# Performance work log

Hardware: AMD Instinct MI355X
Metric: run time of the kernel (lower is better)

Reference implementation:

```python
import jax, jax.numpy as jnp
import numpy as np

HIDDEN = 768
NUM_HEADS = 12
HEAD_SIZE = HIDDEN // NUM_HEADS
LN_EPS = 1e-5


def setup_inputs() -> dict:
    key = jax.random.key(0)
    ks = jax.random.split(key, 10)
    B, S, H = 2, 4096, HIDDEN
    std = 1.0 / np.sqrt(H)
    inp = {
        "hidden_states": jax.random.normal(ks[0], (B, S, H), dtype=jnp.float32),
        "attention_mask": jnp.ones((B, S), dtype=jnp.float32),
        "Wq": jax.random.normal(ks[1], (H, H), dtype=jnp.float32) * std,
        "bq": jnp.zeros((H,), dtype=jnp.float32),
        "Wk": jax.random.normal(ks[2], (H, H), dtype=jnp.float32) * std,
        "bk": jnp.zeros((H,), dtype=jnp.float32),
        "Wv": jax.random.normal(ks[3], (H, H), dtype=jnp.float32) * std,
        "bv": jnp.zeros((H,), dtype=jnp.float32),
        "Wo": jax.random.normal(ks[4], (H, H), dtype=jnp.float32) * std,
        "bo": jnp.zeros((H,), dtype=jnp.float32),
        "ln_gamma": jnp.ones((H,), dtype=jnp.float32),
        "ln_beta": jnp.zeros((H,), dtype=jnp.float32),
    }
    return inp


def _split_heads(x):
    # [B, S, H] -> [B, nH, S, hd]
    B, S, _ = x.shape
    return x.reshape(B, S, NUM_HEADS, HEAD_SIZE).transpose(0, 2, 1, 3)


def reference(hidden_states, attention_mask, Wq, bq, Wk, bk, Wv, bv, Wo, bo, ln_gamma, ln_beta):
    # QKV projections (torch Linear: x @ W.T + b; here W is stored as [in, out])
    q = _split_heads(hidden_states @ Wq + bq)
    k = _split_heads(hidden_states @ Wk + bk)
    v = _split_heads(hidden_states @ Wv + bv)

    scores = jnp.einsum("bhqd,bhkd->bhqk", q, k) / jnp.sqrt(jnp.float32(HEAD_SIZE))
    # additive mask: (1 - mask) * -10000, broadcast over heads and query positions
    scores = scores + (1.0 - attention_mask)[:, None, None, :] * -10000.0
    probs = jax.nn.softmax(scores, axis=-1)  # dropout_prob = 0 -> identity

    ctx = jnp.einsum("bhqk,bhkd->bhqd", probs, v)
    B, _, S, _ = ctx.shape
    ctx = ctx.transpose(0, 2, 1, 3).reshape(B, S, HIDDEN)

    out = ctx @ Wo + bo
    resid = out + hidden_states
    mu = jnp.mean(resid, axis=-1, keepdims=True)
    var = jnp.var(resid, axis=-1, keepdims=True)
    return (resid - mu) * jax.lax.rsqrt(var + LN_EPS) * ln_gamma + ln_beta
```

## Files before the change

### kernel.cpp

```cpp
#include <hip/hip_runtime.h>
#include <hip/hip_bf16.h>

#define HID 768
#define NHEADS 12
#define HDIM 64
#define SEQ 4096
#define BB 2
#define MTOT (BB * SEQ)

typedef __attribute__((ext_vector_type(8))) short bf16x8;
typedef __attribute__((ext_vector_type(16))) float f32x16;

#define LOG2E 1.4426950408889634f

__device__ inline unsigned pack2bf(float a, float b) {
    __hip_bfloat162 h = __float22bfloat162_rn(float2{a, b});
    return *(unsigned*)&h;
}

__global__ __launch_bounds__(256) void cast_x_kernel(
    const float* __restrict__ X, __hip_bfloat16* __restrict__ Xb)
{
    const size_t i = ((size_t)blockIdx.x * 256 + threadIdx.x) * 8;
    const float4 x0 = *(const float4*)(X + i);
    const float4 x1 = *(const float4*)(X + i + 4);
    unsigned u[4];
    u[0] = pack2bf(x0.x, x0.y);
    u[1] = pack2bf(x0.z, x0.w);
    u[2] = pack2bf(x1.x, x1.y);
    u[3] = pack2bf(x1.z, x1.w);
    *(uint4*)(Xb + i) = *(uint4*)u;
}

__global__ __launch_bounds__(256) void pack_w_kernel(
    const float* __restrict__ Wq, const float* __restrict__ Wk,
    const float* __restrict__ Wv, const float* __restrict__ Wo,
    __hip_bfloat16* __restrict__ Wt)
{
    const int z = blockIdx.z;
    const float* __restrict__ W = (z == 0) ? Wq : (z == 1) ? Wk : (z == 2) ? Wv : Wo;
    const int in0  = blockIdx.x * 64;
    const int out0 = blockIdx.y * 64;
    const int t = threadIdx.x;

    __shared__ float T[64][65];
#pragma unroll
    for (int i = 0; i < 4; ++i) {
        const int idx = t + 256 * i;
        const int row = idx >> 4;
        const int c4  = (idx & 15) << 2;
        const float4 v = *(const float4*)(W + (size_t)(in0 + row) * HID + out0 + c4);
        T[row][c4 + 0] = v.x; T[row][c4 + 1] = v.y;
        T[row][c4 + 2] = v.z; T[row][c4 + 3] = v.w;
    }
    __syncthreads();

    const int o  = t >> 2;
    const int cb = (t & 3) << 4;
    __hip_bfloat16 tmp[16];
#pragma unroll
    for (int k = 0; k < 16; ++k)
        tmp[k] = __float2bfloat16(T[cb + k][o]);
    __hip_bfloat16* __restrict__ dst =
        Wt + (size_t)(z * HID + out0 + o) * HID + in0 + cb;
    *(uint4*)(dst)     = *(uint4*)(&tmp[0]);
    *(uint4*)(dst + 8) = *(uint4*)(&tmp[8]);
}

__global__ __launch_bounds__(256) void qkv_mfma_kernel(
    const __hip_bfloat16* __restrict__ Xb, const __hip_bfloat16* __restrict__ Wt,
    const float* __restrict__ bq, const float* __restrict__ bk,
    const float* __restrict__ bv,
    __hip_bfloat16* __restrict__ Qo, __hip_bfloat16* __restrict__ Ko,
    __hip_bfloat16* __restrict__ Vo)
{
    const int nblk = blockIdx.x;
    const int z  = nblk / 6;
    const int f0 = (nblk % 6) * 128;
    const int n0 = nblk * 128;
    const int m0 = blockIdx.y * 128;

    const float* __restrict__ bias = (z == 0) ? bq : (z == 1) ? bk : bv;

    const int t    = threadIdx.x;
    const int w    = t >> 6;
    const int lane = t & 63;
    const int col  = lane & 31;
    const int g    = lane >> 5;
    const int wm   = w & 1;
    const int wn   = w >> 1;

    __shared__ __hip_bfloat16 smem[2 * 128 * 72];
    __hip_bfloat16 (*As)[72] = (__hip_bfloat16(*)[72])smem;
    __hip_bfloat16 (*Bs)[72] = (__hip_bfloat16(*)[72])(smem + 128 * 72);

    f32x16 acc[2][2];
#pragma unroll
    for (int mt = 0; mt < 2; ++mt)
#pragma unroll
        for (int nt = 0; nt < 2; ++nt)
#pragma unroll
            for (int r = 0; r < 16; ++r) acc[mt][nt][r] = 0.f;

    for (int k0 = 0; k0 < HID; k0 += 64) {
        __syncthreads();
#pragma unroll
        for (int i = 0; i < 4; ++i) {
            const int idx = t + 256 * i;
            const int row = idx >> 3;
            const int c8  = (idx & 7) << 3;
            *(uint4*)&As[row][c8] = *(const uint4*)(Xb + (size_t)(m0 + row) * HID + k0 + c8);
            *(uint4*)&Bs[row][c8] = *(const uint4*)(Wt + (size_t)(n0 + row) * HID + k0 + c8);
        }
        __syncthreads();
#pragma unroll
        for (int kh = 0; kh < 4; ++kh) {
            const int ko = 16 * kh + 8 * g;
            const bf16x8 a0 = *(const bf16x8*)&As[64 * wm + col][ko];
            const bf16x8 a1 = *(const bf16x8*)&As[64 * wm + 32 + col][ko];
            const bf16x8 b0 = *(const bf16x8*)&Bs[64 * wn + col][ko];
            const bf16x8 b1 = *(const bf16x8*)&Bs[64 * wn + 32 + col][ko];
            acc[0][0] = __builtin_amdgcn_mfma_f32_32x32x16_bf16(a0, b0, acc[0][0], 0, 0, 0);
            acc[0][1] = __builtin_amdgcn_mfma_f32_32x32x16_bf16(a0, b1, acc[0][1], 0, 0, 0);
            acc[1][0] = __builtin_amdgcn_mfma_f32_32x32x16_bf16(a1, b0, acc[1][0], 0, 0, 0);
            acc[1][1] = __builtin_amdgcn_mfma_f32_32x32x16_bf16(a1, b1, acc[1][1], 0, 0, 0);
        }
    }

    if (z < 2) {
        __hip_bfloat16* __restrict__ Out = (z == 0) ? Qo : Ko;
        const int h = (f0 >> 6) + wn;
#pragma unroll
        for (int mt = 0; mt < 2; ++mt)
#pragma unroll
            for (int nt = 0; nt < 2; ++nt) {
                const int d = 32 * nt + col;
                const float bsv = bias[f0 + 64 * wn + d];
#pragma unroll
                for (int r = 0; r < 16; ++r) {
                    const int m = m0 + 64 * wm + 32 * mt + (r & 3) + 8 * (r >> 2) + 4 * g;
                    const int b = m >> 12;
                    const int s = m & (SEQ - 1);
                    Out[(((size_t)(b * NHEADS + h)) * SEQ + s) * HDIM + d] =
                        __float2bfloat16(acc[mt][nt][r] + bsv);
                }
            }
    } else {
        __syncthreads();
        __hip_bfloat16 (*Ts)[136] = (__hip_bfloat16(*)[136])smem;
#pragma unroll
        for (int mt = 0; mt < 2; ++mt)
#pragma unroll
            for (int nt = 0; nt < 2; ++nt) {
                const int nloc = 64 * wn + 32 * nt + col;
                const float bsv = bias[f0 + nloc];
#pragma unroll
                for (int rg = 0; rg < 4; ++rg) {
                    const int mbase = 64 * wm + 32 * mt + 8 * rg + 4 * g;
                    unsigned pu[2];
                    pu[0] = pack2bf(acc[mt][nt][4 * rg + 0] + bsv,
                                    acc[mt][nt][4 * rg + 1] + bsv);
                    pu[1] = pack2bf(acc[mt][nt][4 * rg + 2] + bsv,
                                    acc[mt][nt][4 * rg + 3] + bsv);
                    *(uint2*)&Ts[nloc][mbase] = *(uint2*)pu;
                }
            }
        __syncthreads();
        const int nloc = t >> 1;
        const int half = t & 1;
        const int hh = (f0 >> 6) + (nloc >> 6);
        const int d  = nloc & 63;
        const int bb = m0 >> 12;
        const int s0 = m0 & (SEQ - 1);
        __hip_bfloat16* __restrict__ dst =
            Vo + (((size_t)(bb * NHEADS + hh)) * HDIM + d) * SEQ + s0 + 64 * half;
        const __hip_bfloat16* srcp = &Ts[nloc][64 * half];
#pragma unroll
        for (int j = 0; j < 8; ++j)
            *(uint4*)(dst + 8 * j) = *(const uint4*)(srcp + 8 * j);
    }
}

typedef __attribute__((ext_vector_type(2))) unsigned uswap2;

__global__ __launch_bounds__(256, 2) void attn_kernel(
    const __hip_bfloat16* __restrict__ Qb, const __hip_bfloat16* __restrict__ Kb,
    const __hip_bfloat16* __restrict__ Vt, const float* __restrict__ mask,
    __hip_bfloat16* __restrict__ Op, float* __restrict__ lp)
{
    const int bh = blockIdx.y;
    const int b  = bh / NHEADS;
    const int h  = bh - b * NHEADS;
    const int kspan = SEQ / gridDim.z;
    const int kbeg  = blockIdx.z * kspan;

    const int t    = threadIdx.x;
    const int w    = t >> 6;
    const int lane = t & 63;
    const int col  = lane & 31;
    const int g    = lane >> 5;
    const int qw   = blockIdx.x * 256 + 64 * w;

    __shared__ __hip_bfloat16 Ksb[2][64][64];
    __shared__ __hip_bfloat16 Vsb[2][64][64];
    __shared__ float madd[2048];

    const __hip_bfloat16* __restrict__ Qh = Qb + (size_t)bh * SEQ * HDIM;
    const __hip_bfloat16* __restrict__ Kh = Kb + (size_t)bh * SEQ * HDIM;
    const __hip_bfloat16* __restrict__ Vh = Vt + (size_t)bh * HDIM * SEQ;

    for (int j = t; j < kspan; j += 256)
        madd[j] = (1.0f - mask[b * SEQ + kbeg + j]) * (-10000.0f * LOG2E);

    const int r0  = t >> 3;
    const int csw = (((t & 7) ^ (r0 & 7)) << 3);

#define STAGE(BUF, KT) do {                                                        \
    const __hip_bfloat16* gk0_ = Kh + (size_t)((KT) + r0) * HDIM + csw;            \
    const __hip_bfloat16* gk1_ = Kh + (size_t)((KT) + r0 + 32) * HDIM + csw;       \
    const __hip_bfloat16* gv0_ = Vh + (size_t)r0 * SEQ + (KT) + csw;               \
    const __hip_bfloat16* gv1_ = Vh + (size_t)(r0 + 32) * SEQ + (KT) + csw;        \
    __hip_bfloat16* lk_ = &Ksb[BUF][0][0] + w * 512;                               \
    __hip_bfloat16* lv_ = &Vsb[BUF][0][0] + w * 512;                               \
    __builtin_amdgcn_global_load_lds(                                              \
        (const __attribute__((address_space(1))) unsigned*)gk0_,                   \
        (__attribute__((address_space(3))) unsigned*)lk_, 16, 0, 0);               \
    __builtin_amdgcn_global_load_lds(                                              \
        (const __attribute__((address_space(1))) unsigned*)gk1_,                   \
        (__attribute__((address_space(3))) unsigned*)(lk_ + 2048), 16, 0, 0);      \
    __builtin_amdgcn_global_load_lds(                                              \
        (const __attribute__((address_space(1))) unsigned*)gv0_,                   \
        (__attribute__((address_space(3))) unsigned*)lv_, 16, 0, 0);               \
    __builtin_amdgcn_global_load_lds(                                              \
        (const __attribute__((address_space(1))) unsigned*)gv1_,                   \
        (__attribute__((address_space(3))) unsigned*)(lv_ + 2048), 16, 0, 0);      \
} while (0)

    bf16x8 bq[2][4];
#pragma unroll
    for (int mt = 0; mt < 2; ++mt)
#pragma unroll
        for (int kh = 0; kh < 4; ++kh)
            bq[mt][kh] = *(const bf16x8*)(Qh + (size_t)(qw + 32 * mt + col) * HDIM
                                          + 16 * kh + 8 * g);

    f32x16 O[2][2];
    float lac[2] = {0.f, 0.f};
#pragma unroll
    for (int mt = 0; mt < 2; ++mt)
#pragma unroll
        for (int dt = 0; dt < 2; ++dt)
#pragma unroll
            for (int r = 0; r < 16; ++r) O[mt][dt][r] = 0.f;

    const float kscale = 0.125f * LOG2E;

#define ATTN_TILE(BUF, KT0) do {                                                   \
    f32x16 St[2][2];                                                               \
    _Pragma("unroll")                                                              \
    for (int mt = 0; mt < 2; ++mt)                                                 \
        _Pragma("unroll")                                                          \
        for (int nt = 0; nt < 2; ++nt)                                             \
            _Pragma("unroll")                                                      \
            for (int r = 0; r < 16; ++r) St[mt][nt][r] = 0.f;                      \
    _Pragma("unroll")                                                              \
    for (int kh = 0; kh < 4; ++kh) {                                               \
        const int sc = ((2 * kh + g) ^ (col & 7)) << 3;                            \
        const bf16x8 ak0 = *(const bf16x8*)&Ksb[BUF][col][sc];                     \
        const bf16x8 ak1 = *(const bf16x8*)&Ksb[BUF][32 + col][sc];                \
        St[0][0] = __builtin_amdgcn_mfma_f32_32x32x16_bf16(ak0, bq[0][kh], St[0][0], 0, 0, 0); \
        St[1][0] = __builtin_amdgcn_mfma_f32_32x32x16_bf16(ak0, bq[1][kh], St[1][0], 0, 0, 0); \
        St[0][1] = __builtin_amdgcn_mfma_f32_32x32x16_bf16(ak1, bq[0][kh], St[0][1], 0, 0, 0); \
        St[1][1] = __builtin_amdgcn_mfma_f32_32x32x16_bf16(ak1, bq[1][kh], St[1][1], 0, 0, 0); \
    }                                                                              \
    _Pragma("unroll")                                                              \
    for (int mt = 0; mt < 2; ++mt) {                                               \
        unsigned g4x[2][4], g4y[2][4];                                             \
        _Pragma("unroll")                                                          \
        for (int nt = 0; nt < 2; ++nt) {                                           \
            _Pragma("unroll")                                                      \
            for (int b4 = 0; b4 < 4; ++b4) {                                       \
                const float4 mm = *(const float4*)&madd[(KT0) + 32 * nt + 8 * b4 + 4 * g]; \
                const float p0 = __builtin_amdgcn_exp2f(fmaf(St[mt][nt][4 * b4 + 0], kscale, mm.x)); \
                const float p1 = __builtin_amdgcn_exp2f(fmaf(St[mt][nt][4 * b4 + 1], kscale, mm.y)); \
                const float p2 = __builtin_amdgcn_exp2f(fmaf(St[mt][nt][4 * b4 + 2], kscale, mm.z)); \
                const float p3 = __builtin_amdgcn_exp2f(fmaf(St[mt][nt][4 * b4 + 3], kscale, mm.w)); \
                lac[mt] += (p0 + p1) + (p2 + p3);                                  \
                g4x[nt][b4] = pack2bf(p0, p1);                                     \
                g4y[nt][b4] = pack2bf(p2, p3);                                     \
            }                                                                      \
        }                                                                          \
        _Pragma("unroll")                                                          \
        for (int kh = 0; kh < 4; ++kh) {                                           \
            const int nt  = kh >> 1;                                               \
            const int khl = kh & 1;                                                \
            union { unsigned u[4]; bf16x8 v; } au;                                 \
            ATTN_PTRANS(au, g4x[nt][2 * khl], g4x[nt][2 * khl + 1],                \
                            g4y[nt][2 * khl], g4y[nt][2 * khl + 1]);               \
            const int sc = ((2 * kh + g) ^ (col & 7)) << 3;                        \
            const bf16x8 bv0 = *(const bf16x8*)&Vsb[BUF][col][sc];                 \
            const bf16x8 bv1 = *(const bf16x8*)&Vsb[BUF][32 + col][sc];            \
            O[mt][0] = __builtin_amdgcn_mfma_f32_32x32x16_bf16(au.v, bv0, O[mt][0], 0, 0, 0); \
            O[mt][1] = __builtin_amdgcn_mfma_f32_32x32x16_bf16(au.v, bv1, O[mt][1], 0, 0, 0); \
        }                                                                          \
    }                                                                              \
} while (0)

#if __has_builtin(__builtin_amdgcn_permlane32_swap)
#define ATTN_PTRANS(au, lox, hix, loy, hiy) do {                                   \
    uswap2 sx_ = __builtin_amdgcn_permlane32_swap((lox), (hix), false, false);     \
    uswap2 sy_ = __builtin_amdgcn_permlane32_swap((loy), (hiy), false, false);     \
    au.u[0] = sx_[0]; au.u[1] = sy_[0]; au.u[2] = sx_[1]; au.u[3] = sy_[1];        \
} while (0)
#else
#define ATTN_PTRANS(au, lox, hix, loy, hiy) do {                                   \
    const unsigned sxv_ = g ? (lox) : (hix);                                       \
    const unsigned syv_ = g ? (loy) : (hiy);                                       \
    const unsigned rx_ = (unsigned)__shfl_xor((int)sxv_, 32, 64);                  \
    const unsigned ry_ = (unsigned)__shfl_xor((int)syv_, 32, 64);                  \
    if (g) { au.u[0] = rx_;   au.u[1] = ry_;   au.u[2] = (hix); au.u[3] = (hiy); } \
    else   { au.u[0] = (lox); au.u[1] = (loy); au.u[2] = rx_;   au.u[3] = ry_;  }  \
} while (0)
#endif

    STAGE(0, kbeg);
    __syncthreads();

    for (int kt0 = 0; kt0 < kspan; kt0 += 128) {
        STAGE(1, kbeg + kt0 + 64);
        ATTN_TILE(0, kt0);
        __syncthreads();
        if (kt0 + 128 < kspan) STAGE(0, kbeg + kt0 + 128);
        ATTN_TILE(1, kt0 + 64);
        __syncthreads();
    }
#undef STAGE
#undef ATTN_TILE
#undef ATTN_PTRANS

    const size_t opbase = (size_t)blockIdx.z * ((size_t)MTOT * HID);
#pragma unroll
    for (int mt = 0; mt < 2; ++mt) {
        const float l = lac[mt] + __shfl_xor(lac[mt], 32, 64);
        if (g == 0)
            lp[((size_t)blockIdx.z * (BB * NHEADS) + bh) * SEQ + qw + 32 * mt + col] = l;
#pragma unroll
        for (int dt = 0; dt < 2; ++dt)
#pragma unroll
            for (int r = 0; r < 16; ++r) {
                const int q = qw + 32 * mt + (r & 3) + 8 * (r >> 2) + 4 * g;
                const int d = 32 * dt + col;
                Op[opbase + ((size_t)b * SEQ + q) * HID + h * HDIM + d] =
                    __float2bfloat16(O[mt][dt][r]);
            }
    }
}

__global__ __launch_bounds__(256) void combine_kernel(
    const __hip_bfloat16* __restrict__ Op, const float* __restrict__ lp,
    __hip_bfloat16* __restrict__ Ctx, int KS)
{
    const size_t i = ((size_t)blockIdx.x * 256 + threadIdx.x) * 8;
    const int n   = (int)(i % HID);
    const int row = (int)(i / HID);
    const int h = n >> 6;
    const int b = row >> 12;
    const int q = row & (SEQ - 1);
    const int bh = b * NHEADS + h;

    float denom = 0.f;
    float o[8] = {};
    for (int kz = 0; kz < KS; ++kz) {
        denom += lp[((size_t)kz * (BB * NHEADS) + bh) * SEQ + q];
        uint4 u = *(const uint4*)(Op + (size_t)kz * ((size_t)MTOT * HID) + i);
        const __hip_bfloat16* e = (const __hip_bfloat16*)&u;
#pragma unroll
        for (int j = 0; j < 8; ++j) o[j] += __bfloat162float(e[j]);
    }
    const float inv = 1.0f / denom;
    unsigned u[4];
#pragma unroll
    for (int j = 0; j < 4; ++j)
        u[j] = pack2bf(o[2 * j] * inv, o[2 * j + 1] * inv);
    *(uint4*)(Ctx + i) = *(uint4*)u;
}

__global__ __launch_bounds__(256) void out_mfma_kernel(
    const __hip_bfloat16* __restrict__ Cb, const __hip_bfloat16* __restrict__ Wto,
    const float* __restrict__ bo, const float* __restrict__ X,
    float* __restrict__ Resid)
{
    const int n0 = blockIdx.x * 128;
    const int m0 = blockIdx.y * 128;

    const int t    = threadIdx.x;
    const int w    = t >> 6;
    const int lane = t & 63;
    const int col  = lane & 31;
    const int g    = lane >> 5;
    const int wm   = w & 1;
    const int wn   = w >> 1;

    __shared__ __hip_bfloat16 As[128][72];
    __shared__ __hip_bfloat16 Bs[128][72];

    f32x16 acc[2][2];
#pragma unroll
    for (int mt = 0; mt < 2; ++mt)
#pragma unroll
        for (int nt = 0; nt < 2; ++nt)
#pragma unroll
            for (int r = 0; r < 16; ++r) acc[mt][nt][r] = 0.f;

    for (int k0 = 0; k0 < HID; k0 += 64) {
        __syncthreads();
#pragma unroll
        for (int i = 0; i < 4; ++i) {
            const int idx = t + 256 * i;
            const int row = idx >> 3;
            const int c8  = (idx & 7) << 3;
            *(uint4*)&As[row][c8] = *(const uint4*)(Cb  + (size_t)(m0 + row) * HID + k0 + c8);
            *(uint4*)&Bs[row][c8] = *(const uint4*)(Wto + (size_t)(n0 + row) * HID + k0 + c8);
        }
        __syncthreads();
#pragma unroll
        for (int kh = 0; kh < 4; ++kh) {
            const int ko = 16 * kh + 8 * g;
            const bf16x8 a0 = *(const bf16x8*)&As[64 * wm + col][ko];
            const bf16x8 a1 = *(const bf16x8*)&As[64 * wm + 32 + col][ko];
            const bf16x8 b0 = *(const bf16x8*)&Bs[64 * wn + col][ko];
            const bf16x8 b1 = *(const bf16x8*)&Bs[64 * wn + 32 + col][ko];
            acc[0][0] = __builtin_amdgcn_mfma_f32_32x32x16_bf16(a0, b0, acc[0][0], 0, 0, 0);
            acc[0][1] = __builtin_amdgcn_mfma_f32_32x32x16_bf16(a0, b1, acc[0][1], 0, 0, 0);
            acc[1][0] = __builtin_amdgcn_mfma_f32_32x32x16_bf16(a1, b0, acc[1][0], 0, 0, 0);
            acc[1][1] = __builtin_amdgcn_mfma_f32_32x32x16_bf16(a1, b1, acc[1][1], 0, 0, 0);
        }
    }

#pragma unroll
    for (int mt = 0; mt < 2; ++mt)
#pragma unroll
        for (int nt = 0; nt < 2; ++nt) {
            const int n = n0 + 64 * wn + 32 * nt + col;
            const float bsv = bo[n];
#pragma unroll
            for (int r = 0; r < 16; ++r) {
                const int m = m0 + 64 * wm + 32 * mt + (r & 3) + 8 * (r >> 2) + 4 * g;
                Resid[(size_t)m * HID + n] = acc[mt][nt][r] + bsv + X[(size_t)m * HID + n];
            }
        }
}

__global__ __launch_bounds__(256) void ln_kernel(
    const float* __restrict__ Rin, const float* __restrict__ gamma,
    const float* __restrict__ beta, float* __restrict__ Out)
{
    const int row = blockIdx.x;
    const int t   = threadIdx.x;
    const float* __restrict__ x = Rin + (size_t)row * HID;

    const float v0 = x[t];
    const float v1 = x[t + 256];
    const float v2 = x[t + 512];
    float s  = v0 + v1 + v2;
    float s2 = v0 * v0 + v1 * v1 + v2 * v2;
#pragma unroll
    for (int off = 32; off; off >>= 1) {
        s  += __shfl_xor(s,  off, 64);
        s2 += __shfl_xor(s2, off, 64);
    }
    __shared__ float rs[4], rs2[4];
    const int w = t >> 6, lane = t & 63;
    if (lane == 0) { rs[w] = s; rs2[w] = s2; }
    __syncthreads();
    const float tot  = rs[0] + rs[1] + rs[2] + rs[3];
    const float tot2 = rs2[0] + rs2[1] + rs2[2] + rs2[3];
    const float mu   = tot * (1.0f / HID);
    const float var  = tot2 * (1.0f / HID) - mu * mu;
    const float rsig = rsqrtf(var + 1e-5f);

    float* __restrict__ y = Out + (size_t)row * HID;
    y[t]       = (v0 - mu) * rsig * gamma[t]       + beta[t];
    y[t + 256] = (v1 - mu) * rsig * gamma[t + 256] + beta[t + 256];
    y[t + 512] = (v2 - mu) * rsig * gamma[t + 512] + beta[t + 512];
}

extern "C" void kernel_launch(void* const* d_in, const int* in_sizes, int n_in,
                              void* d_out, int out_size, void* d_ws, size_t ws_size,
                              hipStream_t stream)
{
    const float* X     = (const float*)d_in[0];
    const float* mask  = (const float*)d_in[1];
    const float* Wq    = (const float*)d_in[2];
    const float* bq    = (const float*)d_in[3];
    const float* Wk    = (const float*)d_in[4];
    const float* bk    = (const float*)d_in[5];
    const float* Wv    = (const float*)d_in[6];
    const float* bv    = (const float*)d_in[7];
    const float* Wo    = (const float*)d_in[8];
    const float* bo    = (const float*)d_in[9];
    const float* gamma = (const float*)d_in[10];
    const float* beta  = (const float*)d_in[11];
    float* out = (float*)d_out;

    const size_t N = (size_t)MTOT * HID;
    const size_t WTE = (size_t)4 * HID * HID;

    char* p = (char*)d_ws;
    __hip_bfloat16* Xb  = (__hip_bfloat16*)p;  p += 2 * N;
    __hip_bfloat16* Wt  = (__hip_bfloat16*)p;  p += 2 * WTE;
    __hip_bfloat16* Qw  = (__hip_bfloat16*)p;  p += 2 * N;
    __hip_bfloat16* Kw  = (__hip_bfloat16*)p;  p += 2 * N;
    __hip_bfloat16* Vtw = (__hip_bfloat16*)p;  p += 2 * N;
    char* opb = p;
    const size_t fixed = (size_t)(opb - (char*)d_ws);

    const size_t lpsz4 = 4 * (size_t)(BB * NHEADS) * SEQ * sizeof(float);
    const int KS = (ws_size >= fixed + 4 * 2 * N + lpsz4) ? 4 : 2;

    __hip_bfloat16* Op  = (__hip_bfloat16*)opb;
    float* lpt = (float*)(opb + (size_t)KS * 2 * N);
    __hip_bfloat16* Ctxb = Xb;
    float* Rd = (float*)Kw;

    cast_x_kernel<<<(int)(N / 2048), 256, 0, stream>>>(X, Xb);
    pack_w_kernel<<<dim3(12, 12, 4), 256, 0, stream>>>(Wq, Wk, Wv, Wo, Wt);
    qkv_mfma_kernel<<<dim3(18, MTOT / 128), 256, 0, stream>>>(
        Xb, Wt, bq, bk, bv, Qw, Kw, Vtw);
    attn_kernel<<<dim3(SEQ / 256, BB * NHEADS, KS), 256, 0, stream>>>(
        Qw, Kw, Vtw, mask, Op, lpt);
    combine_kernel<<<(int)(N / 2048), 256, 0, stream>>>(Op, lpt, Ctxb, KS);
    out_mfma_kernel<<<dim3(6, MTOT / 128), 256, 0, stream>>>(
        Ctxb, Wt + (size_t)2304 * HID, bo, X, Rd);
    ln_kernel<<<MTOT, 256, 0, stream>>>(Rd, gamma, beta, out);
}
```

Measured before the change: 327.4 us.

## Double-buffer projection GEMM tiles with direct global-to-LDS loads and XOR swizzle

The QKV and output projection GEMMs now stage tiles through two LDS buffers, loading the next k-slice while MFMAs consume the current one. Loads go directly from global memory to LDS via global_load_lds, skipping register staging. An XOR column swizzle replaces row padding to avoid bank conflicts. This doubles LDS use per block, which may reduce occupancy, and relies on correct wait handling for async LDS loads.

```diff
diff --git a/kernel.cpp b/kernel.cpp
--- a/kernel.cpp
+++ b/kernel.cpp
@@ -67,6 +67,35 @@
     *(uint4*)(dst + 8) = *(uint4*)(&tmp[8]);
 }
 
+#define GSTAGE(ASB, BSB, BUF, APTR, BPTR, K0) do {                                 \
+    _Pragma("unroll")                                                              \
+    for (int j_ = 0; j_ < 4; ++j_) {                                               \
+        const __hip_bfloat16* ga_ = (APTR) + (size_t)(r0 + 32 * j_) * HID + (K0) + csw; \
+        const __hip_bfloat16* gb_ = (BPTR) + (size_t)(r0 + 32 * j_) * HID + (K0) + csw; \
+        __builtin_amdgcn_global_load_lds(                                          \
+            (const __attribute__((address_space(1))) unsigned*)ga_,                \
+            (__attribute__((address_space(3))) unsigned*)(&ASB[BUF][0][0] + (256 * j_ + 64 * w) * 8), 16, 0, 0); \
+        __builtin_amdgcn_global_load_lds(                                          \
+            (const __attribute__((address_space(1))) unsigned*)gb_,                \
+            (__attribute__((address_space(3))) unsigned*)(&BSB[BUF][0][0] + (256 * j_ + 64 * w) * 8), 16, 0, 0); \
+    }                                                                              \
+} while (0)
+
+#define GTILE(ASB, BSB, BUF) do {                                                  \
+    _Pragma("unroll")                                                              \
+    for (int kh = 0; kh < 4; ++kh) {                                               \
+        const int sc = ((2 * kh + g) ^ (col & 7)) << 3;                            \
+        const bf16x8 a0 = *(const bf16x8*)&ASB[BUF][64 * wm + col][sc];            \
+        const bf16x8 a1 = *(const bf16x8*)&ASB[BUF][64 * wm + 32 + col][sc];       \
+        const bf16x8 b0 = *(const bf16x8*)&BSB[BUF][64 * wn + col][sc];            \
+        const bf16x8 b1 = *(const bf16x8*)&BSB[BUF][64 * wn + 32 + col][sc];       \
+        acc[0][0] = __builtin_amdgcn_mfma_f32_32x32x16_bf16(a0, b0, acc[0][0], 0, 0, 0); \
+        acc[0][1] = __builtin_amdgcn_mfma_f32_32x32x16_bf16(a0, b1, acc[0][1], 0, 0, 0); \
+        acc[1][0] = __builtin_amdgcn_mfma_f32_32x32x16_bf16(a1, b0, acc[1][0], 0, 0, 0); \
+        acc[1][1] = __builtin_amdgcn_mfma_f32_32x32x16_bf16(a1, b1, acc[1][1], 0, 0, 0); \
+    }                                                                              \
+} while (0)
+
 __global__ __launch_bounds__(256) void qkv_mfma_kernel(
     const __hip_bfloat16* __restrict__ Xb, const __hip_bfloat16* __restrict__ Wt,
     const float* __restrict__ bq, const float* __restrict__ bk,
@@ -90,9 +119,15 @@
     const int wm   = w & 1;
     const int wn   = w >> 1;
 
-    __shared__ __hip_bfloat16 smem[2 * 128 * 72];
-    __hip_bfloat16 (*As)[72] = (__hip_bfloat16(*)[72])smem;
-    __hip_bfloat16 (*Bs)[72] = (__hip_bfloat16(*)[72])(smem + 128 * 72);
+    __shared__ __hip_bfloat16 smem[4 * 128 * 64];
+    __hip_bfloat16 (*Asb)[128][64] = (__hip_bfloat16(*)[128][64])smem;
+    __hip_bfloat16 (*Bsb)[128][64] = (__hip_bfloat16(*)[128][64])(smem + 2 * 128 * 64);
+
+    const int r0  = t >> 3;
+    const int csw = (((t & 7) ^ (r0 & 7)) << 3);
+
+    const __hip_bfloat16* __restrict__ Am = Xb + (size_t)m0 * HID;
+    const __hip_bfloat16* __restrict__ Bn = Wt + (size_t)n0 * HID;
 
     f32x16 acc[2][2];
 #pragma unroll
@@ -102,29 +137,15 @@
 #pragma unroll
             for (int r = 0; r < 16; ++r) acc[mt][nt][r] = 0.f;
 
-    for (int k0 = 0; k0 < HID; k0 += 64) {
-        __syncthreads();
-#pragma unroll
-        for (int i = 0; i < 4; ++i) {
-            const int idx = t + 256 * i;
-            const int row = idx >> 3;
-            const int c8  = (idx & 7) << 3;
-            *(uint4*)&As[row][c8] = *(const uint4*)(Xb + (size_t)(m0 + row) * HID + k0 + c8);
-            *(uint4*)&Bs[row][c8] = *(const uint4*)(Wt + (size_t)(n0 + row) * HID + k0 + c8);
-        }
-        __syncthreads();
-#pragma unroll
-        for (int kh = 0; kh < 4; ++kh) {
-            const int ko = 16 * kh + 8 * g;
-            const bf16x8 a0 = *(const bf16x8*)&As[64 * wm + col][ko];
-            const bf16x8 a1 = *(const bf16x8*)&As[64 * wm + 32 + col][ko];
-            const bf16x8 b0 = *(const bf16x8*)&Bs[64 * wn + col][ko];
-            const bf16x8 b1 = *(const bf16x8*)&Bs[64 * wn + 32 + col][ko];
-            acc[0][0] = __builtin_amdgcn_mfma_f32_32x32x16_bf16(a0, b0, acc[0][0], 0, 0, 0);
-            acc[0][1] = __builtin_amdgcn_mfma_f32_32x32x16_bf16(a0, b1, acc[0][1], 0, 0, 0);
-            acc[1][0] = __builtin_amdgcn_mfma_f32_32x32x16_bf16(a1, b0, acc[1][0], 0, 0, 0);
-            acc[1][1] = __builtin_amdgcn_mfma_f32_32x32x16_bf16(a1, b1, acc[1][1], 0, 0, 0);
-        }
+    GSTAGE(Asb, Bsb, 0, Am, Bn, 0);
+    __syncthreads();
+    for (int k0 = 0; k0 < HID; k0 += 128) {
+        GSTAGE(Asb, Bsb, 1, Am, Bn, k0 + 64);
+        GTILE(Asb, Bsb, 0);
+        __syncthreads();
+        if (k0 + 128 < HID) GSTAGE(Asb, Bsb, 0, Am, Bn, k0 + 128);
+        GTILE(Asb, Bsb, 1);
+        __syncthreads();
     }
 
     if (z < 2) {
@@ -401,8 +422,15 @@
     const int wm   = w & 1;
     const int wn   = w >> 1;
 
-    __shared__ __hip_bfloat16 As[128][72];
-    __shared__ __hip_bfloat16 Bs[128][72];
+    __shared__ __hip_bfloat16 smem[4 * 128 * 64];
+    __hip_bfloat16 (*Asb)[128][64] = (__hip_bfloat16(*)[128][64])smem;
+    __hip_bfloat16 (*Bsb)[128][64] = (__hip_bfloat16(*)[128][64])(smem + 2 * 128 * 64);
+
+    const int r0  = t >> 3;
+    const int csw = (((t & 7) ^ (r0 & 7)) << 3);
+
+    const __hip_bfloat16* __restrict__ Am = Cb  + (size_t)m0 * HID;
+    const __hip_bfloat16* __restrict__ Bn = Wto + (size_t)n0 * HID;
 
     f32x16 acc[2][2];
 #pragma unroll
@@ -412,29 +440,15 @@
 #pragma unroll
             for (int r = 0; r < 16; ++r) acc[mt][nt][r] = 0.f;
 
-    for (int k0 = 0; k0 < HID; k0 += 64) {
-        __syncthreads();
-#pragma unroll
-        for (int i = 0; i < 4; ++i) {
-            const int idx = t + 256 * i;
-            const int row = idx >> 3;
-            const int c8  = (idx & 7) << 3;
-            *(uint4*)&As[row][c8] = *(const uint4*)(Cb  + (size_t)(m0 + row) * HID + k0 + c8);
-            *(uint4*)&Bs[row][c8] = *(const uint4*)(Wto + (size_t)(n0 + row) * HID + k0 + c8);
-        }
-        __syncthreads();
-#pragma unroll
-        for (int kh = 0; kh < 4; ++kh) {
-            const int ko = 16 * kh + 8 * g;
-            const bf16x8 a0 = *(const bf16x8*)&As[64 * wm + col][ko];
-            const bf16x8 a1 = *(const bf16x8*)&As[64 * wm + 32 + col][ko];
-            const bf16x8 b0 = *(const bf16x8*)&Bs[64 * wn + col][ko];
-            const bf16x8 b1 = *(const bf16x8*)&Bs[64 * wn + 32 + col][ko];
-            acc[0][0] = __builtin_amdgcn_mfma_f32_32x32x16_bf16(a0, b0, acc[0][0], 0, 0, 0);
-            acc[0][1] = __builtin_amdgcn_mfma_f32_32x32x16_bf16(a0, b1, acc[0][1], 0, 0, 0);
-            acc[1][0] = __builtin_amdgcn_mfma_f32_32x32x16_bf16(a1, b0, acc[1][0], 0, 0, 0);
-            acc[1][1] = __builtin_amdgcn_mfma_f32_32x32x16_bf16(a1, b1, acc[1][1], 0, 0, 0);
-        }
+    GSTAGE(Asb, Bsb, 0, Am, Bn, 0);
+    __syncthreads();
+    for (int k0 = 0; k0 < HID; k0 += 128) {
+        GSTAGE(Asb, Bsb, 1, Am, Bn, k0 + 64);
+        GTILE(Asb, Bsb, 0);
+        __syncthreads();
+        if (k0 + 128 < HID) GSTAGE(Asb, Bsb, 0, Am, Bn, k0 + 128);
+        GTILE(Asb, Bsb, 1);
+        __syncthreads();
     }
 
 #pragma unroll
```

New measurement: 328.1 us. About the same (+0.2%).
